# Kernel optimization log

Hardware: AMD Instinct MI355X
Metric: run time of the kernel (lower is better)

Reference implementation:

```python
import jax, jax.numpy as jnp
import numpy as np

B, L, D_IN, D_MODEL, D_STATE, N_LAYERS = 16, 2048, 64, 512, 16, 4
LN_EPS = 1e-5


def setup_inputs() -> dict:
    key = jax.random.key(0)
    ks = jax.random.split(key, 16)
    s = 0.02
    x = jax.random.normal(ks[0], (B, L, D_IN), jnp.float32)
    W_in0 = jax.random.normal(ks[1], (D_IN, D_MODEL), jnp.float32) * s
    b_in0 = jnp.zeros((D_MODEL,), jnp.float32)
    W_in = jax.random.normal(ks[2], (N_LAYERS - 1, D_MODEL, D_MODEL), jnp.float32) * s
    b_in = jnp.zeros((N_LAYERS - 1, D_MODEL), jnp.float32)
    # S4D-style init: A_log = log(1..N) per channel
    A_log = jnp.broadcast_to(jnp.log(jnp.arange(1, D_STATE + 1, dtype=jnp.float32)), (N_LAYERS, D_MODEL, D_STATE)).copy()
    D_skip = jnp.ones((N_LAYERS, D_MODEL), jnp.float32)
    W_dt = jax.random.normal(ks[3], (N_LAYERS, D_MODEL, D_MODEL), jnp.float32) * s
    b_dt = jnp.full((N_LAYERS, D_MODEL), -4.0, jnp.float32)  # small initial dt
    W_B = jax.random.normal(ks[4], (N_LAYERS, D_MODEL, D_STATE), jnp.float32) * s
    W_C = jax.random.normal(ks[5], (N_LAYERS, D_MODEL, D_STATE), jnp.float32) * s
    ln_g = jnp.ones((D_MODEL,), jnp.float32)
    ln_b = jnp.zeros((D_MODEL,), jnp.float32)
    head_w = jax.random.normal(ks[6], (D_MODEL, 1), jnp.float32) * s
    head_b = jnp.zeros((1,), jnp.float32)
    return {"x": x, "W_in0": W_in0, "b_in0": b_in0, "W_in": W_in, "b_in": b_in,
            "A_log": A_log, "D_skip": D_skip, "W_dt": W_dt, "b_dt": b_dt,
            "W_B": W_B, "W_C": W_C, "ln_g": ln_g, "ln_b": ln_b,
            "head_w": head_w, "head_b": head_b}


def _mamba_layer(x, W_in_l, b_in_l, A_log_l, D_l, W_dt_l, b_dt_l, W_B_l, W_C_l):
    # x: (B, L, d_in) -> y: (B, L, D_MODEL)
    u = x @ W_in_l + b_in_l                    # (B, L, D)
    dt = jax.nn.softplus(u @ W_dt_l + b_dt_l)  # (B, L, D)
    Bm = u @ W_B_l                             # (B, L, N)
    Cm = u @ W_C_l                             # (B, L, N)
    A = -jnp.exp(A_log_l)                      # (D, N)

    def step(h, inp):
        dt_t, u_t, B_t, C_t = inp              # (B,D),(B,D),(B,N),(B,N)
        dA = jnp.exp(dt_t[..., None] * A)      # (B, D, N)
        h = dA * h + (dt_t * u_t)[..., None] * B_t[:, None, :]
        y_t = jnp.einsum('bdn,bn->bd', h, C_t)
        return h, y_t

    h0 = jnp.zeros((u.shape[0], u.shape[2], A.shape[1]), u.dtype)
    xs = (jnp.swapaxes(dt, 0, 1), jnp.swapaxes(u, 0, 1),
          jnp.swapaxes(Bm, 0, 1), jnp.swapaxes(Cm, 0, 1))
    _, ys = jax.lax.scan(step, h0, xs)         # ys: (L, B, D)
    return jnp.swapaxes(ys, 0, 1) + u * D_l


def reference(x, W_in0, b_in0, W_in, b_in, A_log, D_skip, W_dt, b_dt, W_B, W_C, ln_g, ln_b, head_w, head_b):
    h = x
    for i in range(N_LAYERS):
        Wi = W_in0 if i == 0 else W_in[i - 1]
        bi = b_in0 if i == 0 else b_in[i - 1]
        h = _mamba_layer(h, Wi, bi, A_log[i], D_skip[i], W_dt[i], b_dt[i], W_B[i], W_C[i])
    # LayerNorm over d_model
    mu = jnp.mean(h, axis=-1, keepdims=True)
    var = jnp.mean(jnp.square(h - mu), axis=-1, keepdims=True)
    h = (h - mu) * jax.lax.rsqrt(var + LN_EPS) * ln_g + ln_b
    return h[:, -1, :] @ head_w + head_b       # (B, 1)
```

## Files before the change

### kernel.cpp

```cpp
#include <hip/hip_runtime.h>
#include <hip/hip_bf16.h>
#include <cstdint>
#include <cstddef>

#define B_SZ    16
#define L_SZ    2048
#define DIN     64
#define DMODEL  512
#define DSTATE  16
#define NLAYERS 4
#define LN_EPS  1e-5f
#define NC      32
#define TCH     (L_SZ / NC)
#define NFULL   1152

typedef __bf16 bf16x8 __attribute__((ext_vector_type(8)));
typedef float  f32x4  __attribute__((ext_vector_type(4)));
typedef unsigned short u16;
typedef unsigned int   u32;

__device__ __forceinline__ u16 f2bf(float f) {
    u32 u = __builtin_bit_cast(u32, f);
    u += 0x7fffu + ((u >> 16) & 1u);
    return (u16)(u >> 16);
}
__device__ __forceinline__ float bf2f(u16 v) {
    u32 u = ((u32)v) << 16;
    return __builtin_bit_cast(float, u);
}

__device__ __forceinline__ void pow16(float q, float* a_) {
    float q2 = q * q, q4 = q2 * q2, q8 = q4 * q4;
    a_[0] = q;        a_[1] = q2;       a_[2] = q2 * q;   a_[3] = q4;
    a_[4] = q4 * q;   a_[5] = q4 * q2;  a_[6] = a_[5] * q; a_[7] = q8;
    a_[8] = q8 * q;   a_[9] = q8 * q2;  a_[10] = a_[9] * q; a_[11] = q8 * q4;
    a_[12] = a_[11] * q; a_[13] = a_[11] * q2; a_[14] = a_[13] * q; a_[15] = q8 * q8;
}

#define LOG2E 1.4426950408889634f

__device__ __forceinline__ void gload16(const void* g, void* l) {
    __builtin_amdgcn_global_load_lds(
        (__attribute__((address_space(1))) void*)(g),
        (__attribute__((address_space(3))) void*)(l), 16, 0, 0);
}

template <int K>
__global__ __launch_bounds__(512) void gemm_fused(
    const u16* __restrict__ A, const u16* __restrict__ BT,
    const float* __restrict__ bias, u16* __restrict__ Cu,
    u16* __restrict__ Cdt, float* __restrict__ Bo, float* __restrict__ Co,
    int M)
{
    constexpr int BM = 128, BK = 64;
    constexpr int NT = K / BK;
    __shared__ u16 As[2][BM * BK];
    __shared__ u16 Bs[2][BM * BK];

    const int tid = threadIdx.x;
    const int wv = tid >> 6, ln = tid & 63;
    const int mb = blockIdx.x & 255, nb = blockIdx.x >> 8;
    const int bm = mb * BM, bn = nb * BM;
    const int wm = (wv >> 1) * 32, wn = (wv & 1) * 64;

    f32x4 acc[2][4];
#pragma unroll
    for (int i = 0; i < 2; ++i)
#pragma unroll
        for (int j = 0; j < 4; ++j) acc[i][j] = (f32x4){0.f, 0.f, 0.f, 0.f};

    auto stage = [&](int buf, int k0) {
#pragma unroll
        for (int i = 0; i < 2; ++i) {
            int t = i * 512 + tid;
            int m = t >> 3, s = t & 7;
            int ksrc = (s ^ (m & 7)) * 8;
            gload16(A + (size_t)(bm + m) * K + k0 + ksrc,
                    &As[buf][(i * 512 + wv * 64) * 8]);
            gload16(BT + (size_t)(bn + m) * K + k0 + ksrc,
                    &Bs[buf][(i * 512 + wv * 64) * 8]);
        }
    };

    stage(0, 0);
    if (NT > 1) stage(1, BK);

#pragma unroll
    for (int kt = 0; kt < NT; ++kt) {
        if (kt == NT - 1) asm volatile("s_waitcnt vmcnt(0)" ::: "memory");
        else              asm volatile("s_waitcnt vmcnt(4)" ::: "memory");
        __builtin_amdgcn_s_barrier();

        const int buf = kt & 1;
#pragma unroll
        for (int ks = 0; ks < 2; ++ks) {
            bf16x8 af[2], bfr[4];
            const int g = ln >> 4, lm = ln & 15;
            const int c = ks * 4 + g;
#pragma unroll
            for (int e = 0; e < 2; ++e) {
                int ml = wm + e * 16 + lm;
                af[e] = *(const bf16x8*)&As[buf][ml * 64 + ((c ^ (ml & 7)) * 8)];
            }
#pragma unroll
            for (int f = 0; f < 4; ++f) {
                int nl = wn + f * 16 + lm;
                bfr[f] = *(const bf16x8*)&Bs[buf][nl * 64 + ((c ^ (nl & 7)) * 8)];
            }
#pragma unroll
            for (int e = 0; e < 2; ++e)
#pragma unroll
                for (int f = 0; f < 4; ++f)
                    acc[e][f] = __builtin_amdgcn_mfma_f32_16x16x32_bf16(
                        bfr[f], af[e], acc[e][f], 0, 0, 0);
        }

        asm volatile("s_waitcnt lgkmcnt(0)" ::: "memory");
        __builtin_amdgcn_s_barrier();
        if (kt + 2 < NT) stage(buf, (kt + 2) * BK);
    }

    const int cg = ln >> 4, lm = ln & 15;
#pragma unroll
    for (int e = 0; e < 2; ++e) {
        const int rowm = bm + wm + e * 16 + lm;
#pragma unroll
        for (int f = 0; f < 4; ++f) {
            const int nc0 = bn + wn + f * 16 + cg * 4;
            if (bn < DMODEL) {
                float4 bv = *(const float4*)&bias[nc0];
                ushort4 o;
                o.x = f2bf(acc[e][f][0] + bv.x);
                o.y = f2bf(acc[e][f][1] + bv.y);
                o.z = f2bf(acc[e][f][2] + bv.z);
                o.w = f2bf(acc[e][f][3] + bv.w);
                *(ushort4*)&Cu[(size_t)rowm * DMODEL + nc0] = o;
            } else if (bn < 2 * DMODEL) {
                float4 bv = *(const float4*)&bias[nc0];
                float v0 = acc[e][f][0] + bv.x, v1 = acc[e][f][1] + bv.y;
                float v2 = acc[e][f][2] + bv.z, v3 = acc[e][f][3] + bv.w;
                v0 = (v0 > 20.f) ? v0 : __logf(1.f + __expf(v0));
                v1 = (v1 > 20.f) ? v1 : __logf(1.f + __expf(v1));
                v2 = (v2 > 20.f) ? v2 : __logf(1.f + __expf(v2));
                v3 = (v3 > 20.f) ? v3 : __logf(1.f + __expf(v3));
                ushort4 o;
                o.x = f2bf(v0); o.y = f2bf(v1); o.z = f2bf(v2); o.w = f2bf(v3);
                *(ushort4*)&Cdt[(size_t)rowm * DMODEL + (nc0 - DMODEL)] = o;
            } else {
                if (nc0 < 2 * DMODEL + DSTATE) {
                    float4 bv = *(const float4*)&bias[nc0];
                    float4 o;
                    o.x = acc[e][f][0] + bv.x; o.y = acc[e][f][1] + bv.y;
                    o.z = acc[e][f][2] + bv.z; o.w = acc[e][f][3] + bv.w;
                    *(float4*)&Bo[(size_t)rowm * DSTATE + (nc0 - 2 * DMODEL)] = o;
                } else if (nc0 < 2 * DMODEL + 2 * DSTATE) {
                    float4 bv = *(const float4*)&bias[nc0];
                    float4 o;
                    o.x = acc[e][f][0] + bv.x; o.y = acc[e][f][1] + bv.y;
                    o.z = acc[e][f][2] + bv.z; o.w = acc[e][f][3] + bv.w;
                    *(float4*)&Co[(size_t)rowm * DSTATE + (nc0 - 2 * DMODEL - DSTATE)] = o;
                }
            }
        }
    }
}

__global__ __launch_bounds__(256) void wtrans(
    const float* __restrict__ W, u16* __restrict__ WT, int K, int N,
    size_t inStride, size_t outStride)
{
    __shared__ float tile[32][33];
    const float* Wm = W + (size_t)blockIdx.z * inStride;
    u16* WTm = WT + (size_t)blockIdx.z * outStride;
    int k0 = blockIdx.x * 32, n0 = blockIdx.y * 32;
    int tx = threadIdx.x & 31, ty = threadIdx.x >> 5;
#pragma unroll
    for (int i = 0; i < 4; ++i)
        tile[ty + 8 * i][tx] = Wm[(size_t)(k0 + ty + 8 * i) * N + n0 + tx];
    __syncthreads();
#pragma unroll
    for (int i = 0; i < 4; ++i)
        WTm[(size_t)(n0 + ty + 8 * i) * K + k0 + tx] = f2bf(tile[tx][ty + 8 * i]);
}

__global__ __launch_bounds__(256) void wcombo(
    const float* __restrict__ Win, const float* __restrict__ Wr,
    u16* __restrict__ outT, int KD, int wrRow,
    size_t winStride, size_t wrStride, size_t outStride)
{
    __shared__ float wi[16][516];
    __shared__ float wd[512][16];
    const float* WinL = Win + (size_t)blockIdx.z * winStride;
    const float* WrL  = Wr  + (size_t)blockIdx.z * wrStride;
    u16* outL = outT + (size_t)blockIdx.z * outStride;
    const int k0 = blockIdx.x * 16, n0 = blockIdx.y * 16;
    const int tid = threadIdx.x;
    for (int i = tid; i < 16 * 128; i += 256) {
        int r = i >> 7, c = i & 127;
        *(float4*)&wi[r][c * 4] =
            *(const float4*)&WinL[(size_t)(k0 + r) * DMODEL + c * 4];
    }
    for (int i = tid; i < 512 * 4; i += 256) {
        int j = i >> 2, c = i & 3;
        *(float4*)&wd[j][c * 4] =
            *(const float4*)&WrL[(size_t)j * wrRow + n0 + c * 4];
    }
    __syncthreads();
    const int kk = tid & 15, nn = tid >> 4;
    float acc = 0.f;
#pragma unroll 8
    for (int j = 0; j < 512; ++j)
        acc = fmaf(wi[kk][j], wd[j][nn], acc);
    outL[(size_t)(n0 + nn) * KD + k0 + kk] = f2bf(acc);
}

__global__ __launch_bounds__(256) void biasprep(
    const float* __restrict__ bin, const float* __restrict__ Wdt,
    const float* __restrict__ WB, const float* __restrict__ WC,
    const float* __restrict__ bdt, float* __restrict__ biascat,
    size_t binStride, size_t wdtStride, size_t wbcStride,
    size_t bdtStride, size_t outStride)
{
    const float* binL = bin + (size_t)blockIdx.z * binStride;
    const float* WdtL = Wdt + (size_t)blockIdx.z * wdtStride;
    const float* WBL  = WB  + (size_t)blockIdx.z * wbcStride;
    const float* WCL  = WC  + (size_t)blockIdx.z * wbcStride;
    const float* bdtL = bdt + (size_t)blockIdx.z * bdtStride;
    float* outL = biascat + (size_t)blockIdx.z * outStride;
    int idx = blockIdx.x * 256 + threadIdx.x;
    if (idx >= NFULL) return;
    float v;
    if (idx < DMODEL) {
        v = binL[idx];
    } else if (idx < 2 * DMODEL) {
        int n = idx - DMODEL;
        v = bdtL[n];
        for (int j = 0; j < DMODEL; ++j)
            v = fmaf(binL[j], WdtL[(size_t)j * DMODEL + n], v);
    } else if (idx < 2 * DMODEL + DSTATE) {
        int n = idx - 2 * DMODEL;
        v = 0.f;
        for (int j = 0; j < DMODEL; ++j)
            v = fmaf(binL[j], WBL[(size_t)j * DSTATE + n], v);
    } else if (idx < 2 * DMODEL + 2 * DSTATE) {
        int n = idx - 2 * DMODEL - DSTATE;
        v = 0.f;
        for (int j = 0; j < DMODEL; ++j)
            v = fmaf(binL[j], WCL[(size_t)j * DSTATE + n], v);
    } else {
        v = 0.f;
    }
    outL[idx] = v;
}

__global__ __launch_bounds__(256) void castx(
    const float* __restrict__ x, u16* __restrict__ xb, int n4)
{
    int i = blockIdx.x * 256 + threadIdx.x;
    if (i < n4) {
        float4 v = ((const float4*)x)[i];
        ushort4 o;
        o.x = f2bf(v.x); o.y = f2bf(v.y); o.z = f2bf(v.z); o.w = f2bf(v.w);
        ((ushort4*)xb)[i] = o;
    }
}

__global__ __launch_bounds__(256) void scan_pass1(
    const u16* __restrict__ u, const u16* __restrict__ dt,
    const float* __restrict__ Bm, const float* __restrict__ A_log,
    float* __restrict__ P, float* __restrict__ S, float* __restrict__ Q)
{
    const int tid = threadIdx.x;
    const int d = blockIdx.x * 256 + tid;
    const int c = blockIdx.y, b = blockIdx.z;
    __shared__ float Bs[TCH][DSTATE];

    const float* Bsrc = Bm + ((size_t)b * L_SZ + (size_t)c * TCH) * DSTATE;
    for (int i = tid; i < TCH * DSTATE / 4; i += 256)
        ((float4*)Bs)[i] = ((const float4*)Bsrc)[i];

    float Ac[16];
#pragma unroll
    for (int n = 0; n < 16; ++n) Ac[n] = -__expf(A_log[d * DSTATE + n]);
    bool geo = true;
#pragma unroll
    for (int n = 1; n < 16; ++n)
        geo &= fabsf(Ac[n] - (n + 1) * Ac[0]) <= 1e-4f * (n + 1) * fabsf(Ac[0]);
    __syncthreads();

    float s[16];
#pragma unroll
    for (int n = 0; n < 16; ++n) s[n] = 0.f;

    const size_t base = ((size_t)b * L_SZ + (size_t)c * TCH) * DMODEL + d;
    size_t o = (((size_t)b * NC + c) * DMODEL + d) * DSTATE;

    if (geo) {
        const float cK = Ac[0] * LOG2E;
        float qp = 1.f;
#pragma unroll 2
        for (int t = 0; t < TCH; ++t) {
            float dtv = bf2f(dt[base + (size_t)t * DMODEL]);
            float uv  = bf2f(u [base + (size_t)t * DMODEL]);
            float du = dtv * uv;
            float q = exp2f(dtv * cK);
            qp *= q;
            float a_[16];
            pow16(q, a_);
#pragma unroll
            for (int n = 0; n < 16; ++n)
                s[n] = fmaf(a_[n], s[n], du * Bs[t][n]);
        }
        Q[((size_t)b * NC + c) * DMODEL + d] = qp;
#pragma unroll
        for (int n = 0; n < 16; ++n) S[o + n] = s[n];
    } else {
        float p[16];
#pragma unroll
        for (int n = 0; n < 16; ++n) p[n] = 1.f;
#pragma unroll 2
        for (int t = 0; t < TCH; ++t) {
            float dtv = bf2f(dt[base + (size_t)t * DMODEL]);
            float uv  = bf2f(u [base + (size_t)t * DMODEL]);
            float du = dtv * uv;
#pragma unroll
            for (int n = 0; n < 16; ++n) {
                float a = __expf(dtv * Ac[n]);
                p[n] *= a;
                s[n] = fmaf(a, s[n], du * Bs[t][n]);
            }
        }
#pragma unroll
        for (int n = 0; n < 16; ++n) { P[o + n] = p[n]; S[o + n] = s[n]; }
    }
}

__global__ __launch_bounds__(256) void scan_fix(
    const float* __restrict__ P, const float* __restrict__ S,
    const float* __restrict__ Q, const float* __restrict__ A_log,
    float* __restrict__ H0)
{
    const int idx = blockIdx.x * 256 + threadIdx.x;
    const int dn = idx & (DMODEL * DSTATE - 1);
    const int b = idx >> 13;
    const int d = dn >> 4, n = dn & 15;

    float Ac0 = -__expf(A_log[d * DSTATE + 0]);
    bool geo = true;
#pragma unroll
    for (int j = 1; j < 16; ++j) {
        float Acj = -__expf(A_log[d * DSTATE + j]);
        geo &= fabsf(Acj - (j + 1) * Ac0) <= 1e-4f * (j + 1) * fabsf(Ac0);
    }

    float h = 0.f;
#pragma unroll
    for (int c = 0; c < NC; ++c) {
        size_t o = (((size_t)b * NC + c) << 13) + dn;
        H0[o] = h;
        float p;
        if (geo) {
            float base = Q[((size_t)b * NC + c) * DMODEL + d];
            p = 1.f;
            int e = n + 1;
#pragma unroll
            for (int i = 0; i < 5; ++i) {
                if (e & 1) p *= base;
                base *= base;
                e >>= 1;
            }
        } else {
            p = P[o];
        }
        h = fmaf(p, h, S[o]);
    }
}

__global__ __launch_bounds__(256) void scan_pass2(
    const u16* __restrict__ u, const u16* __restrict__ dt,
    const float* __restrict__ Bm, const float* __restrict__ Cm,
    const float* __restrict__ A_log, const float* __restrict__ Dskip,
    const float* __restrict__ H0, u16* __restrict__ yb,
    float* __restrict__ ylast)
{
    const int tid = threadIdx.x;
    const int d = blockIdx.x * 256 + tid;
    const int c = blockIdx.y, b = blockIdx.z;
    __shared__ float Bs[TCH][DSTATE];
    __shared__ float Cs[TCH][DSTATE];

    const float* Bsrc = Bm + ((size_t)b * L_SZ + (size_t)c * TCH) * DSTATE;
    const float* Csrc = Cm + ((size_t)b * L_SZ + (size_t)c * TCH) * DSTATE;
    for (int i = tid; i < TCH * DSTATE / 4; i += 256) {
        ((float4*)Bs)[i] = ((const float4*)Bsrc)[i];
        ((float4*)Cs)[i] = ((const float4*)Csrc)[i];
    }

    float Ac[16];
#pragma unroll
    for (int n = 0; n < 16; ++n) Ac[n] = -__expf(A_log[d * DSTATE + n]);
    bool geo = true;
#pragma unroll
    for (int n = 1; n < 16; ++n)
        geo &= fabsf(Ac[n] - (n + 1) * Ac[0]) <= 1e-4f * (n + 1) * fabsf(Ac[0]);
    const float Dk = Dskip[d];

    float h[16];
    size_t ho = (((size_t)b * NC + c) * DMODEL + d) * DSTATE;
#pragma unroll
    for (int n = 0; n < 16; ++n) h[n] = H0[ho + n];
    __syncthreads();

    const size_t base = ((size_t)b * L_SZ + (size_t)c * TCH) * DMODEL + d;

    if (geo) {
        const float cK = Ac[0] * LOG2E;
#pragma unroll 2
        for (int t = 0; t < TCH; ++t) {
            float dtv = bf2f(dt[base + (size_t)t * DMODEL]);
            float uv  = bf2f(u [base + (size_t)t * DMODEL]);
            float du = dtv * uv;
            float q = exp2f(dtv * cK);
            float a_[16];
            pow16(q, a_);
            float yv = 0.f;
#pragma unroll
            for (int n = 0; n < 16; ++n) {
                h[n] = fmaf(a_[n], h[n], du * Bs[t][n]);
                yv = fmaf(h[n], Cs[t][n], yv);
            }
            yv = fmaf(uv, Dk, yv);
            yb[base + (size_t)t * DMODEL] = f2bf(yv);
            if (c == NC - 1 && t == TCH - 1) ylast[(size_t)b * DMODEL + d] = yv;
        }
    } else {
#pragma unroll 2
        for (int t = 0; t < TCH; ++t) {
            float dtv = bf2f(dt[base + (size_t)t * DMODEL]);
            float uv  = bf2f(u [base + (size_t)t * DMODEL]);
            float du = dtv * uv;
            float yv = 0.f;
#pragma unroll
            for (int n = 0; n < 16; ++n) {
                float a = __expf(dtv * Ac[n]);
                h[n] = fmaf(a, h[n], du * Bs[t][n]);
                yv = fmaf(h[n], Cs[t][n], yv);
            }
            yv = fmaf(uv, Dk, yv);
            yb[base + (size_t)t * DMODEL] = f2bf(yv);
            if (c == NC - 1 && t == TCH - 1) ylast[(size_t)b * DMODEL + d] = yv;
        }
    }
}

__global__ __launch_bounds__(256) void ln_head_kernel(
    const float* __restrict__ ylast, const float* __restrict__ g,
    const float* __restrict__ bb, const float* __restrict__ hw,
    const float* __restrict__ hb, float* __restrict__ out)
{
    const int b = blockIdx.x;
    const int tid = threadIdx.x;
    const float* row = ylast + (size_t)b * DMODEL;
    float v0 = row[tid], v1 = row[tid + 256];
    float s = v0 + v1;
    float s2 = v0 * v0 + v1 * v1;
#pragma unroll
    for (int o = 32; o >= 1; o >>= 1) {
        s += __shfl_xor(s, o);
        s2 += __shfl_xor(s2, o);
    }
    __shared__ float red[8];
    const int w = tid >> 6;
    if ((tid & 63) == 0) { red[w] = s; red[4 + w] = s2; }
    __syncthreads();
    s = red[0] + red[1] + red[2] + red[3];
    s2 = red[4] + red[5] + red[6] + red[7];
    float mu = s * (1.f / DMODEL);
    float var = s2 * (1.f / DMODEL) - mu * mu;
    float r = rsqrtf(var + LN_EPS);
    float c = ((v0 - mu) * r * g[tid] + bb[tid]) * hw[tid]
            + ((v1 - mu) * r * g[tid + 256] + bb[tid + 256]) * hw[tid + 256];
#pragma unroll
    for (int o = 32; o >= 1; o >>= 1) c += __shfl_xor(c, o);
    __syncthreads();
    if ((tid & 63) == 0) red[w] = c;
    __syncthreads();
    if (tid == 0) out[b] = red[0] + red[1] + red[2] + red[3] + hb[0];
}

extern "C" void kernel_launch(void* const* d_in, const int* in_sizes, int n_in,
                              void* d_out, int out_size, void* d_ws, size_t ws_size,
                              hipStream_t stream)
{
    const float* x      = (const float*)d_in[0];
    const float* W_in0  = (const float*)d_in[1];
    const float* b_in0  = (const float*)d_in[2];
    const float* W_in   = (const float*)d_in[3];
    const float* b_in   = (const float*)d_in[4];
    const float* A_log  = (const float*)d_in[5];
    const float* D_skip = (const float*)d_in[6];
    const float* W_dt   = (const float*)d_in[7];
    const float* b_dt   = (const float*)d_in[8];
    const float* W_B    = (const float*)d_in[9];
    const float* W_C    = (const float*)d_in[10];
    const float* ln_g   = (const float*)d_in[11];
    const float* ln_b   = (const float*)d_in[12];
    const float* head_w = (const float*)d_in[13];
    const float* head_b = (const float*)d_in[14];
    float* out = (float*)d_out;

    const size_t BLD = (size_t)B_SZ * L_SZ * DMODEL;
    const size_t BLN = (size_t)B_SZ * L_SZ * DSTATE;
    const size_t BCD = (size_t)B_SZ * NC * DMODEL * DSTATE;
    const size_t BCDQ = (size_t)B_SZ * NC * DMODEL;
    const size_t XBN = (size_t)B_SZ * L_SZ * DIN;

    float* fp = (float*)d_ws;
    float* Bbuf  = fp; fp += BLN;
    float* Cbuf  = fp; fp += BLN;
    float* Pbuf  = fp; fp += BCD;
    float* Sbuf  = fp; fp += BCD;
    float* H0buf = fp; fp += BCD;
    float* Qbuf  = fp; fp += BCDQ;
    float* ylast = fp; fp += (size_t)B_SZ * DMODEL;
    float* biascat = fp; fp += (size_t)NLAYERS * NFULL;
    u16* hp = (u16*)fp;
    u16* xb    = hp; hp += XBN;
    u16* ub    = hp; hp += BLD;
    u16* dtb   = hp; hp += BLD;
    u16* ybuf  = hp; hp += BLD;
    u16* BT0   = hp; hp += (size_t)NFULL * DIN;
    u16* BTcat = hp; hp += (size_t)(NLAYERS - 1) * NFULL * DMODEL;

    const int M = B_SZ * L_SZ;
    const size_t WDM = (size_t)DMODEL * DMODEL;
    const size_t WBN = (size_t)DMODEL * DSTATE;

    hipMemsetAsync(BT0, 0,
        ((size_t)NFULL * DIN + (size_t)(NLAYERS - 1) * NFULL * DMODEL) * sizeof(u16),
        stream);
    castx<<<(XBN / 4 + 255) / 256, 256, 0, stream>>>(x, xb, XBN / 4);
    wtrans<<<dim3(DIN / 32, DMODEL / 32, 1), 256, 0, stream>>>(
        W_in0, BT0, DIN, DMODEL, 0, 0);
    wcombo<<<dim3(DIN / 16, DMODEL / 16, 1), 256, 0, stream>>>(
        W_in0, W_dt, BT0 + (size_t)DMODEL * DIN, DIN, DMODEL, 0, 0, 0);
    wcombo<<<dim3(DIN / 16, 1, 1), 256, 0, stream>>>(
        W_in0, W_B, BT0 + (size_t)2 * DMODEL * DIN, DIN, DSTATE, 0, 0, 0);
    wcombo<<<dim3(DIN / 16, 1, 1), 256, 0, stream>>>(
        W_in0, W_C, BT0 + ((size_t)2 * DMODEL + DSTATE) * DIN, DIN, DSTATE, 0, 0, 0);
    biasprep<<<dim3(5, 1, 1), 256, 0, stream>>>(
        b_in0, W_dt, W_B, W_C, b_dt, biascat, 0, 0, 0, 0, 0);
    wtrans<<<dim3(DMODEL / 32, DMODEL / 32, NLAYERS - 1), 256, 0, stream>>>(
        W_in, BTcat, DMODEL, DMODEL, WDM, (size_t)NFULL * DMODEL);
    wcombo<<<dim3(DMODEL / 16, DMODEL / 16, NLAYERS - 1), 256, 0, stream>>>(
        W_in, W_dt + WDM, BTcat + (size_t)DMODEL * DMODEL, DMODEL, DMODEL,
        WDM, WDM, (size_t)NFULL * DMODEL);
    wcombo<<<dim3(DMODEL / 16, 1, NLAYERS - 1), 256, 0, stream>>>(
        W_in, W_B + WBN, BTcat + (size_t)2 * DMODEL * DMODEL, DMODEL, DSTATE,
        WDM, WBN, (size_t)NFULL * DMODEL);
    wcombo<<<dim3(DMODEL / 16, 1, NLAYERS - 1), 256, 0, stream>>>(
        W_in, W_C + WBN, BTcat + ((size_t)2 * DMODEL + DSTATE) * DMODEL, DMODEL,
        DSTATE, WDM, WBN, (size_t)NFULL * DMODEL);
    biasprep<<<dim3(5, 1, NLAYERS - 1), 256, 0, stream>>>(
        b_in, W_dt + WDM, W_B + WBN, W_C + WBN, b_dt + DMODEL, biascat + NFULL,
        DMODEL, WDM, WBN, DMODEL, NFULL);

    for (int l = 0; l < NLAYERS; ++l) {
        if (l == 0) {
            gemm_fused<DIN><<<(M / 128) * (NFULL / 128), 512, 0, stream>>>(
                xb, BT0, biascat, ub, dtb, Bbuf, Cbuf, M);
        } else {
            gemm_fused<DMODEL><<<(M / 128) * (NFULL / 128), 512, 0, stream>>>(
                ybuf, BTcat + (size_t)(l - 1) * NFULL * DMODEL,
                biascat + (size_t)l * NFULL, ub, dtb, Bbuf, Cbuf, M);
        }
        const float* Al = A_log + (size_t)l * DMODEL * DSTATE;
        scan_pass1<<<dim3(DMODEL / 256, NC, B_SZ), 256, 0, stream>>>(
            ub, dtb, Bbuf, Al, Pbuf, Sbuf, Qbuf);
        scan_fix<<<(B_SZ * DMODEL * DSTATE) / 256, 256, 0, stream>>>(
            Pbuf, Sbuf, Qbuf, Al, H0buf);
        scan_pass2<<<dim3(DMODEL / 256, NC, B_SZ), 256, 0, stream>>>(
            ub, dtb, Bbuf, Cbuf, Al, D_skip + (size_t)l * DMODEL,
            H0buf, ybuf, ylast);
    }

    ln_head_kernel<<<B_SZ, 256, 0, stream>>>(ylast, ln_g, ln_b, head_w, head_b, out);
}
```

Measured before the change: 764.7 us.

## Halve GEMM K-tile, scalarize epilogue, and move scan chunk-power expansion into pass1

The fused GEMM now uses a 32-wide K tile with one 16-byte global-to-LDS load per thread per operand and a new XOR swizzle. MFMA operand order is swapped, so each lane's accumulator now covers four rows of one column, and the epilogue writes scalar elements instead of vectorized ushort4/float4 stores. Separately, scan_pass1 expands the geometric chunk decay into 16 powers and writes the full P array, and scan_fix drops the Q buffer and its geometric-detection path. The smaller K tile doubles the barrier count per GEMM, and the scalar stores may cut store efficiency. pass1 also writes more P data in exchange for a simpler scan_fix.

```diff
diff --git a/kernel.cpp b/kernel.cpp
--- a/kernel.cpp
+++ b/kernel.cpp
@@ -52,7 +52,7 @@
     u16* __restrict__ Cdt, float* __restrict__ Bo, float* __restrict__ Co,
     int M)
 {
-    constexpr int BM = 128, BK = 64;
+    constexpr int BM = 128, BK = 32;
     constexpr int NT = K / BK;
     __shared__ u16 As[2][BM * BK];
     __shared__ u16 Bs[2][BM * BK];
@@ -69,17 +69,11 @@
 #pragma unroll
         for (int j = 0; j < 4; ++j) acc[i][j] = (f32x4){0.f, 0.f, 0.f, 0.f};
 
+    const int sm = tid >> 2, ss = tid & 3;
+    const int ksrc = (ss ^ ((sm >> 1) & 3)) * 8;
     auto stage = [&](int buf, int k0) {
-#pragma unroll
-        for (int i = 0; i < 2; ++i) {
-            int t = i * 512 + tid;
-            int m = t >> 3, s = t & 7;
-            int ksrc = (s ^ (m & 7)) * 8;
-            gload16(A + (size_t)(bm + m) * K + k0 + ksrc,
-                    &As[buf][(i * 512 + wv * 64) * 8]);
-            gload16(BT + (size_t)(bn + m) * K + k0 + ksrc,
-                    &Bs[buf][(i * 512 + wv * 64) * 8]);
-        }
+        gload16(A + (size_t)(bm + sm) * K + k0 + ksrc, &As[buf][(wv * 64) * 8]);
+        gload16(BT + (size_t)(bn + sm) * K + k0 + ksrc, &Bs[buf][(wv * 64) * 8]);
     };
 
     stage(0, 0);
@@ -88,77 +82,56 @@
 #pragma unroll
     for (int kt = 0; kt < NT; ++kt) {
         if (kt == NT - 1) asm volatile("s_waitcnt vmcnt(0)" ::: "memory");
-        else              asm volatile("s_waitcnt vmcnt(4)" ::: "memory");
+        else              asm volatile("s_waitcnt vmcnt(2)" ::: "memory");
         __builtin_amdgcn_s_barrier();
 
         const int buf = kt & 1;
-#pragma unroll
-        for (int ks = 0; ks < 2; ++ks) {
-            bf16x8 af[2], bfr[4];
-            const int g = ln >> 4, lm = ln & 15;
-            const int c = ks * 4 + g;
-#pragma unroll
-            for (int e = 0; e < 2; ++e) {
-                int ml = wm + e * 16 + lm;
-                af[e] = *(const bf16x8*)&As[buf][ml * 64 + ((c ^ (ml & 7)) * 8)];
-            }
-#pragma unroll
-            for (int f = 0; f < 4; ++f) {
-                int nl = wn + f * 16 + lm;
-                bfr[f] = *(const bf16x8*)&Bs[buf][nl * 64 + ((c ^ (nl & 7)) * 8)];
-            }
-#pragma unroll
-            for (int e = 0; e < 2; ++e)
-#pragma unroll
-                for (int f = 0; f < 4; ++f)
-                    acc[e][f] = __builtin_amdgcn_mfma_f32_16x16x32_bf16(
-                        bfr[f], af[e], acc[e][f], 0, 0, 0);
-        }
+        const int g = ln >> 4, lm = ln & 15;
+        bf16x8 af[2], bfr[4];
+#pragma unroll
+        for (int e = 0; e < 2; ++e) {
+            int ml = wm + e * 16 + lm;
+            af[e] = *(const bf16x8*)&As[buf][ml * 32 + ((g ^ ((ml >> 1) & 3)) * 8)];
+        }
+#pragma unroll
+        for (int f = 0; f < 4; ++f) {
+            int nl = wn + f * 16 + lm;
+            bfr[f] = *(const bf16x8*)&Bs[buf][nl * 32 + ((g ^ ((nl >> 1) & 3)) * 8)];
+        }
+#pragma unroll
+        for (int e = 0; e < 2; ++e)
+#pragma unroll
+            for (int f = 0; f < 4; ++f)
+                acc[e][f] = __builtin_amdgcn_mfma_f32_16x16x32_bf16(
+                    af[e], bfr[f], acc[e][f], 0, 0, 0);
 
         asm volatile("s_waitcnt lgkmcnt(0)" ::: "memory");
         __builtin_amdgcn_s_barrier();
         if (kt + 2 < NT) stage(buf, (kt + 2) * BK);
     }
 
-    const int cg = ln >> 4, lm = ln & 15;
+    const int cg = ln >> 4, lc = ln & 15;
 #pragma unroll
     for (int e = 0; e < 2; ++e) {
-        const int rowm = bm + wm + e * 16 + lm;
 #pragma unroll
         for (int f = 0; f < 4; ++f) {
-            const int nc0 = bn + wn + f * 16 + cg * 4;
-            if (bn < DMODEL) {
-                float4 bv = *(const float4*)&bias[nc0];
-                ushort4 o;
-                o.x = f2bf(acc[e][f][0] + bv.x);
-                o.y = f2bf(acc[e][f][1] + bv.y);
-                o.z = f2bf(acc[e][f][2] + bv.z);
-                o.w = f2bf(acc[e][f][3] + bv.w);
-                *(ushort4*)&Cu[(size_t)rowm * DMODEL + nc0] = o;
-            } else if (bn < 2 * DMODEL) {
-                float4 bv = *(const float4*)&bias[nc0];
-                float v0 = acc[e][f][0] + bv.x, v1 = acc[e][f][1] + bv.y;
-                float v2 = acc[e][f][2] + bv.z, v3 = acc[e][f][3] + bv.w;
-                v0 = (v0 > 20.f) ? v0 : __logf(1.f + __expf(v0));
-                v1 = (v1 > 20.f) ? v1 : __logf(1.f + __expf(v1));
-                v2 = (v2 > 20.f) ? v2 : __logf(1.f + __expf(v2));
-                v3 = (v3 > 20.f) ? v3 : __logf(1.f + __expf(v3));
-                ushort4 o;
-                o.x = f2bf(v0); o.y = f2bf(v1); o.z = f2bf(v2); o.w = f2bf(v3);
-                *(ushort4*)&Cdt[(size_t)rowm * DMODEL + (nc0 - DMODEL)] = o;
-            } else {
-                if (nc0 < 2 * DMODEL + DSTATE) {
-                    float4 bv = *(const float4*)&bias[nc0];
-                    float4 o;
-                    o.x = acc[e][f][0] + bv.x; o.y = acc[e][f][1] + bv.y;
-                    o.z = acc[e][f][2] + bv.z; o.w = acc[e][f][3] + bv.w;
-                    *(float4*)&Bo[(size_t)rowm * DSTATE + (nc0 - 2 * DMODEL)] = o;
-                } else if (nc0 < 2 * DMODEL + 2 * DSTATE) {
-                    float4 bv = *(const float4*)&bias[nc0];
-                    float4 o;
-                    o.x = acc[e][f][0] + bv.x; o.y = acc[e][f][1] + bv.y;
-                    o.z = acc[e][f][2] + bv.z; o.w = acc[e][f][3] + bv.w;
-                    *(float4*)&Co[(size_t)rowm * DSTATE + (nc0 - 2 * DMODEL - DSTATE)] = o;
+            int col = bn + wn + f * 16 + lc;
+            float bv = bias[col];
+#pragma unroll
+            for (int r = 0; r < 4; ++r) {
+                int row = bm + wm + e * 16 + cg * 4 + r;
+                float v = acc[e][f][r] + bv;
+                if (bn < DMODEL) {
+                    Cu[(size_t)row * DMODEL + col] = f2bf(v);
+                } else if (bn < 2 * DMODEL) {
+                    v = (v > 20.f) ? v : __logf(1.f + __expf(v));
+                    Cdt[(size_t)row * DMODEL + (col - DMODEL)] = f2bf(v);
+                } else {
+                    if (col < 2 * DMODEL + DSTATE) {
+                        Bo[(size_t)row * DSTATE + (col - 2 * DMODEL)] = v;
+                    } else if (col < 2 * DMODEL + 2 * DSTATE) {
+                        Co[(size_t)row * DSTATE + (col - 2 * DMODEL - DSTATE)] = v;
+                    }
                 }
             }
         }
@@ -268,7 +241,7 @@
 __global__ __launch_bounds__(256) void scan_pass1(
     const u16* __restrict__ u, const u16* __restrict__ dt,
     const float* __restrict__ Bm, const float* __restrict__ A_log,
-    float* __restrict__ P, float* __restrict__ S, float* __restrict__ Q)
+    float* __restrict__ P, float* __restrict__ S)
 {
     const int tid = threadIdx.x;
     const int d = blockIdx.x * 256 + tid;
@@ -311,9 +284,10 @@
             for (int n = 0; n < 16; ++n)
                 s[n] = fmaf(a_[n], s[n], du * Bs[t][n]);
         }
-        Q[((size_t)b * NC + c) * DMODEL + d] = qp;
-#pragma unroll
-        for (int n = 0; n < 16; ++n) S[o + n] = s[n];
+        float p_[16];
+        pow16(qp, p_);
+#pragma unroll
+        for (int n = 0; n < 16; ++n) { P[o + n] = p_[n]; S[o + n] = s[n]; }
     } else {
         float p[16];
 #pragma unroll
@@ -337,42 +311,17 @@
 
 __global__ __launch_bounds__(256) void scan_fix(
     const float* __restrict__ P, const float* __restrict__ S,
-    const float* __restrict__ Q, const float* __restrict__ A_log,
     float* __restrict__ H0)
 {
     const int idx = blockIdx.x * 256 + threadIdx.x;
     const int dn = idx & (DMODEL * DSTATE - 1);
     const int b = idx >> 13;
-    const int d = dn >> 4, n = dn & 15;
-
-    float Ac0 = -__expf(A_log[d * DSTATE + 0]);
-    bool geo = true;
-#pragma unroll
-    for (int j = 1; j < 16; ++j) {
-        float Acj = -__expf(A_log[d * DSTATE + j]);
-        geo &= fabsf(Acj - (j + 1) * Ac0) <= 1e-4f * (j + 1) * fabsf(Ac0);
-    }
-
     float h = 0.f;
 #pragma unroll
     for (int c = 0; c < NC; ++c) {
         size_t o = (((size_t)b * NC + c) << 13) + dn;
         H0[o] = h;
-        float p;
-        if (geo) {
-            float base = Q[((size_t)b * NC + c) * DMODEL + d];
-            p = 1.f;
-            int e = n + 1;
-#pragma unroll
-            for (int i = 0; i < 5; ++i) {
-                if (e & 1) p *= base;
-                base *= base;
-                e >>= 1;
-            }
-        } else {
-            p = P[o];
-        }
-        h = fmaf(p, h, S[o]);
+        h = fmaf(P[o], h, S[o]);
     }
 }
 
@@ -512,7 +461,6 @@
     const size_t BLD = (size_t)B_SZ * L_SZ * DMODEL;
     const size_t BLN = (size_t)B_SZ * L_SZ * DSTATE;
     const size_t BCD = (size_t)B_SZ * NC * DMODEL * DSTATE;
-    const size_t BCDQ = (size_t)B_SZ * NC * DMODEL;
     const size_t XBN = (size_t)B_SZ * L_SZ * DIN;
 
     float* fp = (float*)d_ws;
@@ -521,7 +469,6 @@
     float* Pbuf  = fp; fp += BCD;
     float* Sbuf  = fp; fp += BCD;
     float* H0buf = fp; fp += BCD;
-    float* Qbuf  = fp; fp += BCDQ;
     float* ylast = fp; fp += (size_t)B_SZ * DMODEL;
     float* biascat = fp; fp += (size_t)NLAYERS * NFULL;
     u16* hp = (u16*)fp;
@@ -576,9 +523,9 @@
         }
         const float* Al = A_log + (size_t)l * DMODEL * DSTATE;
         scan_pass1<<<dim3(DMODEL / 256, NC, B_SZ), 256, 0, stream>>>(
-            ub, dtb, Bbuf, Al, Pbuf, Sbuf, Qbuf);
+            ub, dtb, Bbuf, Al, Pbuf, Sbuf);
         scan_fix<<<(B_SZ * DMODEL * DSTATE) / 256, 256, 0, stream>>>(
-            Pbuf, Sbuf, Qbuf, Al, H0buf);
+            Pbuf, Sbuf, H0buf);
         scan_pass2<<<dim3(DMODEL / 256, NC, B_SZ), 256, 0, stream>>>(
             ub, dtb, Bbuf, Cbuf, Al, D_skip + (size_t)l * DMODEL,
             H0buf, ybuf, ylast);
```

New measurement: 734.3 us. 4.0% less time.
